# Kernel optimization log

Hardware: AMD Instinct MI355X
Metric: run time of the kernel (lower is better)

The kernel has to match this reference:

```python
import jax, jax.numpy as jnp
import numpy as np

EPS = 1e-5
NEG = -1e9

def _ln(x, g, b):
    m = x.mean(-1, keepdims=True)
    v = ((x - m) ** 2).mean(-1, keepdims=True)
    return (x - m) / jnp.sqrt(v + EPS) * g + b

def setup_inputs() -> dict:
    key = jax.random.key(0)
    ks = jax.random.split(key, 32)
    B, N, D, F, L = 2, 512, 128, 512, 3
    s = 0.05
    rn = lambda k, sh, sc=s: jax.random.normal(k, sh, jnp.float32) * sc
    inp = {
        'rel_matrix': rn(ks[0], (B, N, N, 2), 1.0),
        'pre_w': rn(ks[1], (2, D)), 'pre_b': rn(ks[2], (D,)),
        'proj_w': rn(ks[3], (2 * D, D)), 'proj_b': rn(ks[4], (D,)),
        'out_w1': rn(ks[5], (D, D)),
        'bn_g': 1.0 + rn(ks[6], (D,)), 'bn_b': rn(ks[7], (D,)),
        'bn_m': rn(ks[8], (D,)),
        'bn_v': 0.5 + jax.random.uniform(ks[9], (D,), jnp.float32),
        'out_w2': rn(ks[10], (D, D)), 'out_b2': rn(ks[11], (D,)),
        'pe': rn(ks[12], (128, D)),
        'wq': rn(ks[13], (L, D, D)), 'bq': rn(ks[14], (L, D)),
        'wk': rn(ks[15], (L, D, D)), 'bk': rn(ks[16], (L, D)),
        'wv': rn(ks[17], (L, D, D)), 'bv': rn(ks[18], (L, D)),
        'wo': rn(ks[19], (L, D, D)), 'bo': rn(ks[20], (L, D)),
        'ln1g': jnp.ones((L, D), jnp.float32), 'ln1b': jnp.zeros((L, D), jnp.float32),
        'ln2g': jnp.ones((L, D), jnp.float32), 'ln2b': jnp.zeros((L, D), jnp.float32),
        'fw1': rn(ks[21], (L, D, F)), 'fb1': rn(ks[22], (L, F)),
        'fw2': rn(ks[23], (L, F, D)), 'fb2': rn(ks[24], (L, D)),
        'mask': jax.random.randint(ks[25], (B, N), 0, 2) > 0,
        'agent_id': jax.random.randint(ks[26], (B, N), 0, 128, dtype=jnp.int32),
    }
    return inp

def reference(rel_matrix, pre_w, pre_b, proj_w, proj_b, out_w1, bn_g, bn_b, bn_m, bn_v,
              out_w2, out_b2, pe, wq, bq, wk, bk, wv, bv, wo, bo,
              ln1g, ln1b, ln2g, ln2b, fw1, fb1, fw2, fb2, mask, agent_id):
    # --- pairwise relation chain (the headroom target) ---
    # symmetric pairwise validity mask (B,N,N)
    pm = (mask[:, None, :] & mask[:, :, None]).astype(rel_matrix.dtype)
    count = jnp.maximum(pm.sum(axis=2), 1.0)  # (B,N) valid-partner counts
    x = rel_matrix @ pre_w + pre_b            # (B,N,N,D) pre_proj Linear(2->128)
    pooled = jnp.einsum('bijd,bij->bid', x, pm) / count[..., None]  # masked mean over j
    x = jnp.concatenate([x, jnp.broadcast_to(pooled[:, :, None, :], x.shape)], axis=-1)
    x = x @ proj_w + proj_b                   # Linear(256->128)
    x = jnp.einsum('bijd,bij->bid', x, pm) / count[..., None]       # masked mean over j
    # out MLP: Linear(no bias) + BatchNorm1d(eval) + ReLU + Linear
    h = x @ out_w1
    h = (h - bn_m) / jnp.sqrt(bn_v + EPS) * bn_g + bn_b
    x = jax.nn.relu(h) @ out_w2 + out_b2
    x = x + pe[agent_id]                      # agent positional embedding
    # --- 3 post-norm single-head transformer layers (eval, dropout off) ---
    kbias = jnp.where(mask, 0.0, NEG)[:, None, :]  # key padding bias (B,1,N)
    scale = 1.0 / jnp.sqrt(jnp.asarray(x.shape[-1], x.dtype))
    for l in range(3):
        q = x @ wq[l] + bq[l]
        k = x @ wk[l] + bk[l]
        v = x @ wv[l] + bv[l]
        a = jax.nn.softmax(jnp.einsum('bid,bjd->bij', q, k) * scale + kbias, axis=-1)
        att = jnp.einsum('bij,bjd->bid', a, v) @ wo[l] + bo[l]
        x = _ln(x + att, ln1g[l], ln1b[l])
        ff = jax.nn.relu(x @ fw1[l] + fb1[l]) @ fw2[l] + fb2[l]
        x = _ln(x + ff, ln2g[l], ln2b[l])
    return x
```

## Files before the change

kernel.cpp:

```cpp
#include <hip/hip_runtime.h>
#include <hip/hip_bf16.h>

typedef unsigned short u16;
typedef unsigned int u32;
typedef unsigned char u8;
typedef __attribute__((ext_vector_type(8))) short bf16x8;
typedef __attribute__((ext_vector_type(4))) float f32x4;

#define DEV __device__ __forceinline__

DEV float bf2f(u16 u) { union { u32 i; float f; } c; c.i = ((u32)u) << 16; return c.f; }
DEV u16 f2bf(float f) {
  union { float f; u32 i; } c; c.f = f;
  u32 r = c.i + 0x7FFFu + ((c.i >> 16) & 1u);
  return (u16)(r >> 16);
}
DEV u32 pk2(float lo, float hi) { return (u32)f2bf(lo) | ((u32)f2bf(hi) << 16); }
DEV float rdsrc(const void* p, int e, int isb) {
  return isb ? bf2f(((const u16*)p)[e]) : ((const float*)p)[e];
}
DEV bf16x8 as_bf(uint4 v) { union { uint4 u; bf16x8 h; } c; c.u = v; return c.h; }

static constexpr int B = 2, N = 512, D = 128, F = 512;
static constexpr int NROW = B * N;
static constexpr float EPS = 1e-5f;
static constexpr float NEG = -1e9f;
static constexpr float SCALE = 0.08838834764831845f;

#define OFF_PRE_W   0
#define OFF_PRE_B   256
#define OFF_PROJ_B  33152
#define OFF_BN_G    49664
#define OFF_BN_B    49792
#define OFF_BN_M    49920
#define OFF_BN_V    50048
#define OFF_OUT_B2  66560
#define OFF_PE      66688
#define OFF_BQ      132224
#define OFF_BK      181760
#define OFF_BV      231296
#define OFF_BO      280832
#define OFF_LN1G    281216
#define OFF_LN1B    281600
#define OFF_LN2G    281984
#define OFF_LN2B    282368
#define OFF_FB1     479360
#define OFF_FB2     677504
#define W_TOTAL     677888

static constexpr int PB_PROJ = 0;
static constexpr int PB_OW1  = 8192;
static constexpr int PB_OW2  = 16384;
static constexpr int PB_L0   = 24576;
static constexpr int PB_LSTR = 98304;
static constexpr int PB_WO   = 24576;
static constexpr int PB_FW1  = 32768;
static constexpr int PB_FW2  = 65536;
static constexpr int PTOT    = 79872;

struct NEnt { const void* s; int off, n; };
struct PEnt { const void* s1; const void* s2; int o1, o2, dst, lgn, cum; };
struct PrepArgs { NEnt nrm[19]; PEnt pk[21]; };

template<int KT>
DEV f32x4 mmaKo(const uint4* __restrict__ aPk, const uint4* __restrict__ Bp,
                int ncol, int col, int lane, int kt0) {
  f32x4 acc = {0.f, 0.f, 0.f, 0.f};
  const int sub = lane >> 4;
  #pragma unroll
  for (int kt = 0; kt < KT; ++kt) {
    const int e8 = (kt0 + kt) * 4 + sub;
    acc = __builtin_amdgcn_mfma_f32_16x16x32_bf16(
        as_bf(aPk[e8 * 16 + (lane & 15)]),
        as_bf(Bp[(size_t)e8 * ncol + col]),
        acc, 0, 0, 0);
  }
  return acc;
}

DEV void packRD(u32* aPkU, int r, int d, float v) {
  const float p = __shfl_xor(v, 1, 64);
  if (!(d & 1))
    aPkU[(((d >> 3) * 16 + r) << 2) + ((d >> 1) & 3)] = pk2(v, p);
}

DEV void packP16(u32* aPkU, int colbase, int lane, f32x4 v) {
  f32x4 p;
  #pragma unroll
  for (int g = 0; g < 4; ++g) p[g] = __shfl_xor(v[g], 1, 64);
  if (!(lane & 1)) {
    const int c = colbase + lane;
    const int e8 = c >> 3, slot = (c >> 1) & 3;
    #pragma unroll
    for (int g = 0; g < 4; ++g)
      aPkU[((e8 * 16 + g) << 2) + slot] = pk2(v[g], p[g]);
  }
}

__global__ __launch_bounds__(256) void k_prep(PrepArgs pa,
    const void* __restrict__ bnv, const void* __restrict__ maskp,
    int* __restrict__ flags, int* __restrict__ mbuf,
    float* __restrict__ W, u32* __restrict__ Wb)
{
  const int t = threadIdx.x, bid = blockIdx.x;
  __shared__ int s_nb, s_m4, s_m2;
  if (t == 0) { s_nb = 0; s_m4 = 0; s_m2 = 0; }
  __syncthreads();
  if (t < 64) {
    const u32 w = ((const u32*)bnv)[t];
    if (((w >> 8) & 0xFFu) != 0x3Fu || ((w >> 24) & 0xFFu) != 0x3Fu)
      atomicOr(&s_nb, 1);
  }
  __syncthreads();
  const int isb = s_nb ? 0 : 1;

  if (bid < 16) {
    for (int ten = 0; ten < 19; ++ten) {
      const NEnt E = pa.nrm[ten];
      for (int e = bid * 256 + t; e < E.n; e += 16 * 256)
        W[E.off + e] = rdsrc(E.s, e, isb);
    }
  } else if (bid < 511) {
    for (int g = (bid - 16) * 256 + t; g < PTOT; g += 495 * 256) {
      int ei = 0;
      #pragma unroll
      for (int k = 1; k < 21; ++k) if (g >= pa.pk[k].cum) ei = k;
      const PEnt E = pa.pk[ei];
      const int li = g - E.cum;
      const int e8 = li >> E.lgn, c = li & ((1 << E.lgn) - 1);
      float f[8];
      #pragma unroll
      for (int i = 0; i < 8; ++i) {
        const int si = ((e8 * 8 + i) << E.lgn) + c;
        f[i] = rdsrc(E.s1, E.o1 + si, isb);
        if (E.s2) f[i] += rdsrc(E.s2, E.o2 + si, isb);
      }
      uint4 w;
      w.x = pk2(f[0], f[1]); w.y = pk2(f[2], f[3]);
      w.z = pk2(f[4], f[5]); w.w = pk2(f[6], f[7]);
      ((uint4*)(Wb + E.dst))[li] = w;
    }
  } else {
    {
      const u32 w = ((const u32*)maskp)[t];
      if (!(w == 0u || w == 1u || w == 0x3F800000u)) atomicOr(&s_m4, 1);
      if (!(w == 0u || w == 1u || w == 0x10000u || w == 0x10001u ||
            w == 0x3F80u || w == 0x3F800000u || w == 0x3F803F80u)) atomicOr(&s_m2, 1);
    }
    __syncthreads();
    const int mode = (!s_m4) ? 4 : ((!s_m2) ? 2 : 1);
    if (t == 0) { flags[0] = isb; flags[1] = mode; }
    #pragma unroll
    for (int k = 0; k < 4; ++k) {
      const int e = k * 256 + t;
      int v;
      if (mode == 4)      v = (((const u32*)maskp)[e] != 0u);
      else if (mode == 2) v = (((const u16*)maskp)[e] != 0);
      else                v = (((const u8*)maskp)[e]  != 0);
      mbuf[e] = v;
    }
  }
}

__global__ __launch_bounds__(512) void k_relq(
    const void* __restrict__ relv, const float* __restrict__ W,
    const u32* __restrict__ Wb,
    const int* __restrict__ flags, const int* __restrict__ mbuf,
    const int* __restrict__ agent_id, float* __restrict__ xbuf,
    float* __restrict__ qb, u32* __restrict__ kbT, u32* __restrict__ vbT)
{
  const int t = threadIdx.x;
  const int row0 = blockIdx.x * 4;
  const int b = row0 >> 9;
  const int wid = t >> 6;
  const int lane = t & 63;

  __shared__ uint4 aPk[2][256];
  __shared__ float wred[8][9];
  __shared__ float sT0[4], sT1[4], sMt;

  u32* a0 = (u32*)&aPk[0][0];
  u32* a1 = (u32*)&aPk[1][0];

  float s0[4] = {0, 0, 0, 0}, s1[4] = {0, 0, 0, 0}, cnt;
  {
    const int j = t;
    const float m = (float)mbuf[b * N + j];
    cnt = m;
    if (flags[0]) {
      const u32* rel2 = (const u32*)relv;
      #pragma unroll
      for (int r = 0; r < 4; ++r) {
        const u32 u = rel2[(size_t)(row0 + r) * N + j];
        s0[r] += m * bf2f((u16)(u & 0xFFFFu));
        s1[r] += m * bf2f((u16)(u >> 16));
      }
    } else {
      const float2* relf = (const float2*)relv;
      #pragma unroll
      for (int r = 0; r < 4; ++r) {
        const float2 u = relf[(size_t)(row0 + r) * N + j];
        s0[r] += m * u.x; s1[r] += m * u.y;
      }
    }
  }
  if ((t & 15) >= 4) {
    const uint4 z = {0u, 0u, 0u, 0u};
    aPk[t >> 8][t & 255] = z;
  }
  #pragma unroll
  for (int o = 32; o > 0; o >>= 1) {
    #pragma unroll
    for (int r = 0; r < 4; ++r) {
      s0[r] += __shfl_xor(s0[r], o, 64);
      s1[r] += __shfl_xor(s1[r], o, 64);
    }
    cnt += __shfl_xor(cnt, o, 64);
  }
  if ((t & 63) == 0) {
    #pragma unroll
    for (int r = 0; r < 4; ++r) { wred[wid][r] = s0[r]; wred[wid][4 + r] = s1[r]; }
    wred[wid][8] = cnt;
  }
  __syncthreads();
  if (t < 4) {
    float a0v = 0, a1v = 0;
    #pragma unroll
    for (int w = 0; w < 8; ++w) { a0v += wred[w][t]; a1v += wred[w][4 + t]; }
    sT0[t] = a0v; sT1[t] = a1v;
  }
  if (t == 8) {
    float c = 0;
    #pragma unroll
    for (int w = 0; w < 8; ++w) c += wred[w][8];
    sMt = c;
  }
  __syncthreads();

  {
    const int r = t >> 7, c = t & 127;
    const int mi = mbuf[row0 + r];
    const float v = mi ? (sT0[r] * W[OFF_PRE_W + c] + sT1[r] * W[OFF_PRE_W + D + c]) / sMt
                         + W[OFF_PRE_B + c]
                       : 0.f;
    packRD(a0, r, c, v);
  }
  __syncthreads();

  {
    const int col = wid * 16 + (lane & 15);
    f32x4 acc = mmaKo<4>(&aPk[0][0], (const uint4*)(Wb + PB_PROJ), 128, col, lane, 0);
    if (lane < 16) {
      const float pb = W[OFF_PROJ_B + col];
      f32x4 v;
      #pragma unroll
      for (int g = 0; g < 4; ++g) v[g] = mbuf[row0 + g] ? acc[g] + pb : 0.f;
      packP16(a1, wid * 16, lane, v);
    }
  }
  __syncthreads();

  {
    const int col = wid * 16 + (lane & 15);
    f32x4 acc = mmaKo<4>(&aPk[1][0], (const uint4*)(Wb + PB_OW1), 128, col, lane, 0);
    if (lane < 16) {
      const float bnm = W[OFF_BN_M + col];
      const float rs  = __frsqrt_rn(W[OFF_BN_V + col] + EPS);
      const float bg  = W[OFF_BN_G + col], bb = W[OFF_BN_B + col];
      f32x4 v;
      #pragma unroll
      for (int g = 0; g < 4; ++g) v[g] = fmaxf((acc[g] - bnm) * rs * bg + bb, 0.f);
      packP16(a0, wid * 16, lane, v);
    }
  }
  __syncthreads();

  {
    const int col = wid * 16 + (lane & 15);
    f32x4 acc = mmaKo<4>(&aPk[0][0], (const uint4*)(Wb + PB_OW2), 128, col, lane, 0);
    if (lane < 16) {
      const float ob = W[OFF_OUT_B2 + col];
      f32x4 v;
      #pragma unroll
      for (int g = 0; g < 4; ++g) {
        const int aid = agent_id[row0 + g];
        v[g] = acc[g] + ob + W[OFF_PE + aid * D + col];
        xbuf[(size_t)(row0 + g) * D + col] = v[g];
      }
      packP16(a1, wid * 16, lane, v);
    }
  }
  __syncthreads();

  {
    const int col = wid * 16 + (lane & 15);
    const int i0 = row0 & 511;
    #pragma unroll
    for (int m = 0; m < 3; ++m) {
      f32x4 acc = mmaKo<4>(&aPk[1][0], (const uint4*)(Wb + PB_L0 + m * 8192), 128, col, lane, 0);
      if (lane < 16) {
        const float bb = W[(m == 0 ? OFF_BQ : m == 1 ? OFF_BK : OFF_BV) + col];
        f32x4 v;
        #pragma unroll
        for (int g = 0; g < 4; ++g) v[g] = acc[g] + bb;
        if (m == 0) {
          #pragma unroll
          for (int g = 0; g < 4; ++g) qb[(size_t)(row0 + g) * D + col] = v[g];
        } else if (m == 1) {
          f32x4 p;
          #pragma unroll
          for (int g = 0; g < 4; ++g) p[g] = __shfl_xor(v[g], 1, 64);
          if (!(lane & 1)) {
            const int e8 = col >> 3, slot = (col >> 1) & 3;
            #pragma unroll
            for (int g = 0; g < 4; ++g)
              ((u32*)kbT)[(((size_t)b * 16 + e8) * 512 + i0 + g) * 4 + slot] = pk2(v[g], p[g]);
          }
        } else {
          uint2 w;
          w.x = pk2(v[0], v[1]); w.y = pk2(v[2], v[3]);
          *(uint2*)(vbT + (((size_t)b * 64 + (i0 >> 3)) * 128 + col) * 4 + 2 * ((i0 >> 2) & 1)) = w;
        }
      }
    }
  }
}

__global__ __launch_bounds__(1024) void k_layer(
    const float* __restrict__ qin, const u32* __restrict__ kinT, const u32* __restrict__ vinT,
    const float* __restrict__ W, const u32* __restrict__ Wb, const int l, const int last,
    float* __restrict__ qout, u32* __restrict__ koutT, u32* __restrict__ voutT,
    const int* __restrict__ mbuf, float* __restrict__ xbuf, float* __restrict__ outp)
{
  const int t = threadIdx.x;
  const int row0 = blockIdx.x * 4;
  const int b = row0 >> 9;
  const int wid = t >> 6;
  const int lane = t & 63;
  const int w8 = wid & 7, half = wid >> 3;

  const uint4* WOp = (const uint4*)(Wb + PB_L0 + l * PB_LSTR + PB_WO);
  const uint4* W1p = (const uint4*)(Wb + PB_L0 + l * PB_LSTR + PB_FW1);
  const uint4* W2p = (const uint4*)(Wb + PB_L0 + l * PB_LSTR + PB_FW2);
  const float* bo  = W + OFF_BO  + l * D;
  const float* g1  = W + OFF_LN1G + l * D;
  const float* b1  = W + OFF_LN1B + l * D;
  const float* fb1 = W + OFF_FB1 + l * F;
  const float* fb2 = W + OFF_FB2 + l * D;
  const float* g2  = W + OFF_LN2G + l * D;
  const float* b2v = W + OFF_LN2B + l * D;

  __shared__ float bufA[4][512];
  __shared__ float xs[4][D];
  __shared__ float pA[4][D], pB[4][D];
  __shared__ uint4 aPk[2][1024];
  __shared__ float den[4];

  u32* a0 = (u32*)&aPk[0][0];
  u32* a1 = (u32*)&aPk[1][0];

  for (int i = t; i < 2048; i += 1024)
    if ((i & 15) >= 4) {
      const uint4 z = {0u, 0u, 0u, 0u};
      aPk[i >> 10][i & 1023] = z;
    }
  if (t < 512) {
    const int r = t >> 7, d = t & 127;
    packRD(a0, r, d, qin[(size_t)(row0 + r) * D + d] * SCALE);
  }
  __syncthreads();

  {
    const uint4* Kp = (const uint4*)kinT + (size_t)b * 16 * 512;
    #pragma unroll
    for (int ii = 0; ii < 2; ++ii) {
      const int col = (wid + 16 * ii) * 16 + (lane & 15);
      f32x4 acc = mmaKo<4>(&aPk[0][0], Kp, 512, col, lane, 0);
      if (lane < 16) {
        const float bias = mbuf[b * N + col] ? 0.f : NEG;
        #pragma unroll
        for (int g = 0; g < 4; ++g) bufA[g][col] = acc[g] + bias;
      }
    }
  }
  __syncthreads();

  if (wid < 4) {
    const int r = wid;
    float pv[8];
    float mx = -1e30f;
    #pragma unroll
    for (int k = 0; k < 8; ++k) { pv[k] = bufA[r][lane + 64 * k]; mx = fmaxf(mx, pv[k]); }
    #pragma unroll
    for (int o = 32; o > 0; o >>= 1) mx = fmaxf(mx, __shfl_xor(mx, o, 64));
    float sum = 0.f;
    #pragma unroll
    for (int k = 0; k < 8; ++k) { pv[k] = __expf(pv[k] - mx); sum += pv[k]; }
    #pragma unroll
    for (int o = 32; o > 0; o >>= 1) sum += __shfl_xor(sum, o, 64);
    #pragma unroll
    for (int k = 0; k < 8; ++k) {
      const float pp = __shfl_xor(pv[k], 1, 64);
      if (!(lane & 1)) {
        const int c = lane + 64 * k;
        a1[(((c >> 3) * 16 + r) << 2) + ((c >> 1) & 3)] = pk2(pv[k], pp);
      }
    }
    if (lane == 0) den[r] = sum;
  }
  __syncthreads();

  {
    const int col = w8 * 16 + (lane & 15);
    const uint4* Vp = (const uint4*)vinT + (size_t)b * 64 * 128;
    f32x4 acc = mmaKo<8>(&aPk[1][0], Vp, 128, col, lane, half * 8);
    if (lane < 16) {
      float* dst = half ? &pB[0][0] : &pA[0][0];
      #pragma unroll
      for (int g = 0; g < 4; ++g) dst[g * D + col] = acc[g];
    }
  }
  __syncthreads();

  if (t < 512) {
    const int r = t >> 7, d = t & 127;
    packRD(a0, r, d, (pA[r][d] + pB[r][d]) / den[r]);
  }
  __syncthreads();

  {
    const int col = w8 * 16 + (lane & 15);
    f32x4 acc = mmaKo<2>(&aPk[0][0], WOp, 128, col, lane, half * 2);
    if (lane < 16) {
      float* dst = half ? &pB[0][0] : &pA[0][0];
      #pragma unroll
      for (int g = 0; g < 4; ++g) dst[g * D + col] = acc[g];
    }
  }
  __syncthreads();

  if (wid < 4) {
    const int r = wid;
    float tv[2];
    #pragma unroll
    for (int k = 0; k < 2; ++k) {
      const int d = lane + 64 * k;
      tv[k] = pA[r][d] + pB[r][d] + bo[d] + xbuf[(size_t)(row0 + r) * D + d];
    }
    float s = tv[0] + tv[1], sq = tv[0] * tv[0] + tv[1] * tv[1];
    #pragma unroll
    for (int o = 32; o > 0; o >>= 1) { s += __shfl_xor(s, o, 64); sq += __shfl_xor(sq, o, 64); }
    const float mean = s * (1.f / 128.f);
    const float var  = sq * (1.f / 128.f) - mean * mean;
    const float rstd = __frsqrt_rn(var + EPS);
    #pragma unroll
    for (int k = 0; k < 2; ++k) {
      const int d = lane + 64 * k;
      const float xn = (tv[k] - mean) * rstd * g1[d] + b1[d];
      xs[r][d] = xn;
      const float pp = __shfl_xor(xn, 1, 64);
      if (!(lane & 1))
        a1[(((d >> 3) * 16 + r) << 2) + ((d >> 1) & 3)] = pk2(xn, pp);
    }
  }
  __syncthreads();

  {
    #pragma unroll
    for (int ii = 0; ii < 2; ++ii) {
      const int colbase = (wid + 16 * ii) * 16;
      const int col = colbase + (lane & 15);
      f32x4 acc = mmaKo<4>(&aPk[1][0], W1p, 512, col, lane, 0);
      if (lane < 16) {
        const float bb = fb1[col];
        f32x4 v;
        #pragma unroll
        for (int g = 0; g < 4; ++g) v[g] = fmaxf(acc[g] + bb, 0.f);
        packP16(a0, colbase, lane, v);
      }
    }
  }
  __syncthreads();

  {
    const int col = w8 * 16 + (lane & 15);
    f32x4 acc = mmaKo<8>(&aPk[0][0], W2p, 128, col, lane, half * 8);
    if (lane < 16) {
      float* dst = half ? &pB[0][0] : &pA[0][0];
      #pragma unroll
      for (int g = 0; g < 4; ++g) dst[g * D + col] = acc[g];
    }
  }
  __syncthreads();

  if (wid < 4) {
    const int r = wid;
    float tv[2];
    #pragma unroll
    for (int k = 0; k < 2; ++k) {
      const int d = lane + 64 * k;
      tv[k] = pA[r][d] + pB[r][d] + fb2[d] + xs[r][d];
    }
    float s = tv[0] + tv[1], sq = tv[0] * tv[0] + tv[1] * tv[1];
    #pragma unroll
    for (int o = 32; o > 0; o >>= 1) { s += __shfl_xor(s, o, 64); sq += __shfl_xor(sq, o, 64); }
    const float mean = s * (1.f / 128.f);
    const float var  = sq * (1.f / 128.f) - mean * mean;
    const float rstd = __frsqrt_rn(var + EPS);
    #pragma unroll
    for (int k = 0; k < 2; ++k) {
      const int d = lane + 64 * k;
      const float xn = (tv[k] - mean) * rstd * g2[d] + b2v[d];
      xbuf[(size_t)(row0 + r) * D + d] = xn;
      if (last) outp[(size_t)(row0 + r) * D + d] = xn;
      const float pp = __shfl_xor(xn, 1, 64);
      if (!last && !(lane & 1))
        a1[(((d >> 3) * 16 + r) << 2) + ((d >> 1) & 3)] = pk2(xn, pp);
    }
  }

  if (!last) {
    __syncthreads();
    const int i0 = row0 & 511;
    #pragma unroll
    for (int it = 0; it < 2; ++it) {
      const int task = wid + 16 * it;
      if (task < 24) {
        const int m = task >> 3, c8 = task & 7;
        const int col = c8 * 16 + (lane & 15);
        const uint4* Bp = (const uint4*)(Wb + PB_L0 + (l + 1) * PB_LSTR + m * 8192);
        f32x4 acc = mmaKo<4>(&aPk[1][0], Bp, 128, col, lane, 0);
        if (lane < 16) {
          const float bb = W[(m == 0 ? OFF_BQ : m == 1 ? OFF_BK : OFF_BV) + (l + 1) * D + col];
          f32x4 v;
          #pragma unroll
          for (int g = 0; g < 4; ++g) v[g] = acc[g] + bb;
          if (m == 0) {
            #pragma unroll
            for (int g = 0; g < 4; ++g) qout[(size_t)(row0 + g) * D + col] = v[g];
          } else if (m == 1) {
            f32x4 p;
            #pragma unroll
            for (int g = 0; g < 4; ++g) p[g] = __shfl_xor(v[g], 1, 64);
            if (!(lane & 1)) {
              const int e8 = col >> 3, slot = (col >> 1) & 3;
              #pragma unroll
              for (int g = 0; g < 4; ++g)
                ((u32*)koutT)[(((size_t)b * 16 + e8) * 512 + i0 + g) * 4 + slot] = pk2(v[g], p[g]);
            }
          } else {
            uint2 w;
            w.x = pk2(v[0], v[1]); w.y = pk2(v[2], v[3]);
            *(uint2*)(voutT + (((size_t)b * 64 + (i0 >> 3)) * 128 + col) * 4 + 2 * ((i0 >> 2) & 1)) = w;
          }
        }
      }
    }
  }
}

extern "C" void kernel_launch(void* const* d_in, const int* in_sizes, int n_in,
                              void* d_out, int out_size, void* d_ws, size_t ws_size,
                              hipStream_t stream) {
  int*   flags = (int*)d_ws;
  int*   mbuf  = flags + 16;
  float* xbuf  = (float*)d_ws + 1040;
  float* q0    = xbuf + NROW * D;
  float* q1    = q0 + NROW * D;
  u32*   kT0   = (u32*)(q1 + NROW * D);
  u32*   kT1   = kT0 + 65536;
  u32*   vT0   = kT1 + 65536;
  u32*   vT1   = vT0 + 65536;
  float* W     = (float*)(vT1 + 65536);
  u32*   Wb    = (u32*)(W + W_TOTAL);

  PrepArgs pa;
  {
    const NEnt nrm[19] = {
      {d_in[1],  OFF_PRE_W,  256}, {d_in[2],  OFF_PRE_B, 128},
      {d_in[4],  OFF_PROJ_B, 128},
      {d_in[6],  OFF_BN_G,   128}, {d_in[7],  OFF_BN_B,  128},
      {d_in[8],  OFF_BN_M,   128}, {d_in[9],  OFF_BN_V,  128},
      {d_in[11], OFF_OUT_B2, 128}, {d_in[12], OFF_PE,  16384},
      {d_in[14], OFF_BQ,     384}, {d_in[16], OFF_BK,    384},
      {d_in[18], OFF_BV,     384}, {d_in[20], OFF_BO,    384},
      {d_in[21], OFF_LN1G,   384}, {d_in[22], OFF_LN1B,  384},
      {d_in[23], OFF_LN2G,   384}, {d_in[24], OFF_LN2B,  384},
      {d_in[26], OFF_FB1,   1536}, {d_in[28], OFF_FB2,   384}};
    for (int i = 0; i < 19; ++i) pa.nrm[i] = nrm[i];

    pa.pk[0] = {d_in[3], d_in[3], 0, 16384, PB_PROJ, 7, 0};
    pa.pk[1] = {d_in[5],  nullptr, 0, 0, PB_OW1, 7, 2048};
    pa.pk[2] = {d_in[10], nullptr, 0, 0, PB_OW2, 7, 4096};
    for (int l = 0; l < 3; ++l) {
      const int lb = PB_L0 + l * PB_LSTR;
      const int cl = 6144 + l * 24576;
      pa.pk[3 + 6 * l + 0] = {d_in[13], nullptr, l * 16384, 0, lb,          7, cl};
      pa.pk[3 + 6 * l + 1] = {d_in[15], nullptr, l * 16384, 0, lb + 8192,   7, cl + 2048};
      pa.pk[3 + 6 * l + 2] = {d_in[17], nullptr, l * 16384, 0, lb + 16384,  7, cl + 4096};
      pa.pk[3 + 6 * l + 3] = {d_in[19], nullptr, l * 16384, 0, lb + PB_WO,  7, cl + 6144};
      pa.pk[3 + 6 * l + 4] = {d_in[25], nullptr, l * 65536, 0, lb + PB_FW1, 9, cl + 8192};
      pa.pk[3 + 6 * l + 5] = {d_in[27], nullptr, l * 65536, 0, lb + PB_FW2, 7, cl + 16384};
    }
  }
  const int* agent_id = (const int*)d_in[30];

  k_prep<<<512, 256, 0, stream>>>(pa, d_in[9], d_in[29], flags, mbuf, W, Wb);
  k_relq<<<NROW / 4, 512, 0, stream>>>(d_in[0], W, Wb, flags, mbuf, agent_id, xbuf,
                                       q0, kT0, vT0);

  float* qs_[2] = {q0, q1};
  u32*   ks_[2] = {kT0, kT1};
  u32*   vs_[2] = {vT0, vT1};
  for (int l = 0; l < 3; ++l) {
    const int cur = l & 1, nxt = cur ^ 1;
    const int last = (l == 2);
    k_layer<<<NROW / 4, 1024, 0, stream>>>(
        qs_[cur], ks_[cur], vs_[cur],
        W, Wb, l, last,
        qs_[nxt], ks_[nxt], vs_[nxt],
        mbuf, xbuf, last ? (float*)d_out : (float*)nullptr);
  }
}
```

Baseline: 66.63 us.

## Prefetch MFMA B operands into registers before barriers and store Q pre-packed bf16

Each matmul stage in the layer kernel now loads its weight, K and V operand fragments into registers before the preceding __syncthreads, so global-load latency overlaps the barrier and the previous stage. Q is written pre-packed in bf16 MFMA layout, so the next layer copies it straight into shared memory instead of converting and packing fp32. The softmax scale is folded into K at write time. This raises register pressure at 1024 threads per block and changes rounding order slightly, since Q and the scaled K are now rounded to bf16 separately.

```diff
diff --git a/kernel.cpp b/kernel.cpp
--- a/kernel.cpp
+++ b/kernel.cpp
@@ -78,6 +78,30 @@
   return acc;
 }
 
+template<int KT>
+DEV void loadB(const uint4* __restrict__ Bp, int ncol, int col, int lane,
+               int kt0, uint4* breg) {
+  const int sub = lane >> 4;
+  #pragma unroll
+  for (int kt = 0; kt < KT; ++kt)
+    breg[kt] = Bp[(size_t)((kt0 + kt) * 4 + sub) * ncol + col];
+}
+
+template<int KT>
+DEV f32x4 mmaR(const uint4* __restrict__ aPk, const uint4* breg, int lane, int kt0) {
+  f32x4 acc = {0.f, 0.f, 0.f, 0.f};
+  const int sub = lane >> 4;
+  #pragma unroll
+  for (int kt = 0; kt < KT; ++kt) {
+    const int e8 = (kt0 + kt) * 4 + sub;
+    acc = __builtin_amdgcn_mfma_f32_16x16x32_bf16(
+        as_bf(aPk[e8 * 16 + (lane & 15)]),
+        as_bf(breg[kt]),
+        acc, 0, 0, 0);
+  }
+  return acc;
+}
+
 DEV void packRD(u32* aPkU, int r, int d, float v) {
   const float p = __shfl_xor(v, 1, 64);
   if (!(d & 1))
@@ -167,10 +191,11 @@
     const u32* __restrict__ Wb,
     const int* __restrict__ flags, const int* __restrict__ mbuf,
     const int* __restrict__ agent_id, float* __restrict__ xbuf,
-    float* __restrict__ qb, u32* __restrict__ kbT, u32* __restrict__ vbT)
+    u32* __restrict__ qP, u32* __restrict__ kbT, u32* __restrict__ vbT)
 {
   const int t = threadIdx.x;
-  const int row0 = blockIdx.x * 4;
+  const int blk = blockIdx.x;
+  const int row0 = blk * 4;
   const int b = row0 >> 9;
   const int wid = t >> 6;
   const int lane = t & 63;
@@ -304,8 +329,15 @@
         #pragma unroll
         for (int g = 0; g < 4; ++g) v[g] = acc[g] + bb;
         if (m == 0) {
+          f32x4 p;
           #pragma unroll
-          for (int g = 0; g < 4; ++g) qb[(size_t)(row0 + g) * D + col] = v[g];
+          for (int g = 0; g < 4; ++g) p[g] = __shfl_xor(v[g], 1, 64);
+          if (!(lane & 1)) {
+            const int e8 = col >> 3, slot = (col >> 1) & 3;
+            #pragma unroll
+            for (int g = 0; g < 4; ++g)
+              qP[blk * 256 + (e8 * 4 + g) * 4 + slot] = pk2(v[g], p[g]);
+          }
         } else if (m == 1) {
           f32x4 p;
           #pragma unroll
@@ -314,7 +346,8 @@
             const int e8 = col >> 3, slot = (col >> 1) & 3;
             #pragma unroll
             for (int g = 0; g < 4; ++g)
-              ((u32*)kbT)[(((size_t)b * 16 + e8) * 512 + i0 + g) * 4 + slot] = pk2(v[g], p[g]);
+              ((u32*)kbT)[(((size_t)b * 16 + e8) * 512 + i0 + g) * 4 + slot]
+                  = pk2(v[g] * SCALE, p[g] * SCALE);
           }
         } else {
           uint2 w;
@@ -327,13 +360,14 @@
 }
 
 __global__ __launch_bounds__(1024) void k_layer(
-    const float* __restrict__ qin, const u32* __restrict__ kinT, const u32* __restrict__ vinT,
+    const u32* __restrict__ qPin, const u32* __restrict__ kinT, const u32* __restrict__ vinT,
     const float* __restrict__ W, const u32* __restrict__ Wb, const int l, const int last,
-    float* __restrict__ qout, u32* __restrict__ koutT, u32* __restrict__ voutT,
+    u32* __restrict__ qPout, u32* __restrict__ koutT, u32* __restrict__ voutT,
     const int* __restrict__ mbuf, float* __restrict__ xbuf, float* __restrict__ outp)
 {
   const int t = threadIdx.x;
-  const int row0 = blockIdx.x * 4;
+  const int blk = blockIdx.x;
+  const int row0 = blk * 4;
   const int b = row0 >> 9;
   const int wid = t >> 6;
   const int lane = t & 63;
@@ -364,18 +398,20 @@
       const uint4 z = {0u, 0u, 0u, 0u};
       aPk[i >> 10][i & 1023] = z;
     }
-  if (t < 512) {
-    const int r = t >> 7, d = t & 127;
-    packRD(a0, r, d, qin[(size_t)(row0 + r) * D + d] * SCALE);
-  }
-  __syncthreads();
-
-  {
-    const uint4* Kp = (const uint4*)kinT + (size_t)b * 16 * 512;
+  if (t < 64)
+    aPk[0][(t >> 2) * 16 + (t & 3)] = ((const uint4*)qPin)[blk * 64 + t];
+  const uint4* Kp = (const uint4*)kinT + (size_t)b * 16 * 512;
+  uint4 kB[2][4];
+  #pragma unroll
+  for (int ii = 0; ii < 2; ++ii)
+    loadB<4>(Kp, 512, (wid + 16 * ii) * 16 + (lane & 15), lane, 0, kB[ii]);
+  __syncthreads();
+
+  {
     #pragma unroll
     for (int ii = 0; ii < 2; ++ii) {
       const int col = (wid + 16 * ii) * 16 + (lane & 15);
-      f32x4 acc = mmaKo<4>(&aPk[0][0], Kp, 512, col, lane, 0);
+      f32x4 acc = mmaR<4>(&aPk[0][0], kB[ii], lane, 0);
       if (lane < 16) {
         const float bias = mbuf[b * N + col] ? 0.f : NEG;
         #pragma unroll
@@ -383,6 +419,9 @@
       }
     }
   }
+  const uint4* Vp = (const uint4*)vinT + (size_t)b * 64 * 128;
+  uint4 vB[8];
+  loadB<8>(Vp, 128, w8 * 16 + (lane & 15), lane, half * 8, vB);
   __syncthreads();
 
   if (wid < 4) {
@@ -412,14 +451,15 @@
 
   {
     const int col = w8 * 16 + (lane & 15);
-    const uint4* Vp = (const uint4*)vinT + (size_t)b * 64 * 128;
-    f32x4 acc = mmaKo<8>(&aPk[1][0], Vp, 128, col, lane, half * 8);
+    f32x4 acc = mmaR<8>(&aPk[1][0], vB, lane, half * 8);
     if (lane < 16) {
       float* dst = half ? &pB[0][0] : &pA[0][0];
       #pragma unroll
       for (int g = 0; g < 4; ++g) dst[g * D + col] = acc[g];
     }
   }
+  uint4 woB[2];
+  loadB<2>(WOp, 128, w8 * 16 + (lane & 15), lane, half * 2, woB);
   __syncthreads();
 
   if (t < 512) {
@@ -430,13 +470,17 @@
 
   {
     const int col = w8 * 16 + (lane & 15);
-    f32x4 acc = mmaKo<2>(&aPk[0][0], WOp, 128, col, lane, half * 2);
+    f32x4 acc = mmaR<2>(&aPk[0][0], woB, lane, half * 2);
     if (lane < 16) {
       float* dst = half ? &pB[0][0] : &pA[0][0];
       #pragma unroll
       for (int g = 0; g < 4; ++g) dst[g * D + col] = acc[g];
     }
   }
+  uint4 w1B[2][4];
+  #pragma unroll
+  for (int ii = 0; ii < 2; ++ii)
+    loadB<4>(W1p, 512, (wid + 16 * ii) * 16 + (lane & 15), lane, 0, w1B[ii]);
   __syncthreads();
 
   if (wid < 4) {
@@ -469,10 +513,9 @@
     #pragma unroll
     for (int ii = 0; ii < 2; ++ii) {
       const int colbase = (wid + 16 * ii) * 16;
-      const int col = colbase + (lane & 15);
-      f32x4 acc = mmaKo<4>(&aPk[1][0], W1p, 512, col, lane, 0);
+      f32x4 acc = mmaR<4>(&aPk[1][0], w1B[ii], lane, 0);
       if (lane < 16) {
-        const float bb = fb1[col];
+        const float bb = fb1[colbase + lane];
         f32x4 v;
         #pragma unroll
         for (int g = 0; g < 4; ++g) v[g] = fmaxf(acc[g] + bb, 0.f);
@@ -480,15 +523,29 @@
       }
     }
   }
+  uint4 w2B[8];
+  loadB<8>(W2p, 128, w8 * 16 + (lane & 15), lane, half * 8, w2B);
   __syncthreads();
 
   {
     const int col = w8 * 16 + (lane & 15);
-    f32x4 acc = mmaKo<8>(&aPk[0][0], W2p, 128, col, lane, half * 8);
+    f32x4 acc = mmaR<8>(&aPk[0][0], w2B, lane, half * 8);
     if (lane < 16) {
       float* dst = half ? &pB[0][0] : &pA[0][0];
       #pragma unroll
       for (int g = 0; g < 4; ++g) dst[g * D + col] = acc[g];
+    }
+  }
+  uint4 jB[2][4];
+  if (!last) {
+    #pragma unroll
+    for (int it = 0; it < 2; ++it) {
+      const int task = wid + 16 * it;
+      if (task < 24) {
+        const int m = task >> 3, c8 = task & 7;
+        const uint4* Bp = (const uint4*)(Wb + PB_L0 + (l + 1) * PB_LSTR + m * 8192);
+        loadB<4>(Bp, 128, c8 * 16 + (lane & 15), lane, 0, jB[it]);
+      }
     }
   }
   __syncthreads();
@@ -528,16 +585,22 @@
       if (task < 24) {
         const int m = task >> 3, c8 = task & 7;
         const int col = c8 * 16 + (lane & 15);
-        const uint4* Bp = (const uint4*)(Wb + PB_L0 + (l + 1) * PB_LSTR + m * 8192);
-        f32x4 acc = mmaKo<4>(&aPk[1][0], Bp, 128, col, lane, 0);
+        f32x4 acc = mmaR<4>(&aPk[1][0], jB[it], lane, 0);
         if (lane < 16) {
           const float bb = W[(m == 0 ? OFF_BQ : m == 1 ? OFF_BK : OFF_BV) + (l + 1) * D + col];
           f32x4 v;
           #pragma unroll
           for (int g = 0; g < 4; ++g) v[g] = acc[g] + bb;
           if (m == 0) {
+            f32x4 p;
             #pragma unroll
-            for (int g = 0; g < 4; ++g) qout[(size_t)(row0 + g) * D + col] = v[g];
+            for (int g = 0; g < 4; ++g) p[g] = __shfl_xor(v[g], 1, 64);
+            if (!(lane & 1)) {
+              const int e8 = col >> 3, slot = (col >> 1) & 3;
+              #pragma unroll
+              for (int g = 0; g < 4; ++g)
+                qPout[blk * 256 + (e8 * 4 + g) * 4 + slot] = pk2(v[g], p[g]);
+            }
           } else if (m == 1) {
             f32x4 p;
             #pragma unroll
@@ -546,7 +609,8 @@
               const int e8 = col >> 3, slot = (col >> 1) & 3;
               #pragma unroll
               for (int g = 0; g < 4; ++g)
-                ((u32*)koutT)[(((size_t)b * 16 + e8) * 512 + i0 + g) * 4 + slot] = pk2(v[g], p[g]);
+                ((u32*)koutT)[(((size_t)b * 16 + e8) * 512 + i0 + g) * 4 + slot]
+                    = pk2(v[g] * SCALE, p[g] * SCALE);
             }
           } else {
             uint2 w;
@@ -565,9 +629,9 @@
   int*   flags = (int*)d_ws;
   int*   mbuf  = flags + 16;
   float* xbuf  = (float*)d_ws + 1040;
-  float* q0    = xbuf + NROW * D;
-  float* q1    = q0 + NROW * D;
-  u32*   kT0   = (u32*)(q1 + NROW * D);
+  u32*   qP0   = (u32*)(xbuf + NROW * D);
+  u32*   qP1   = qP0 + 65536;
+  u32*   kT0   = qP1 + 65536;
   u32*   kT1   = kT0 + 65536;
   u32*   vT0   = kT1 + 65536;
   u32*   vT1   = vT0 + 65536;
@@ -607,11 +671,11 @@
 
   k_prep<<<512, 256, 0, stream>>>(pa, d_in[9], d_in[29], flags, mbuf, W, Wb);
   k_relq<<<NROW / 4, 512, 0, stream>>>(d_in[0], W, Wb, flags, mbuf, agent_id, xbuf,
-                                       q0, kT0, vT0);
-
-  float* qs_[2] = {q0, q1};
-  u32*   ks_[2] = {kT0, kT1};
-  u32*   vs_[2] = {vT0, vT1};
+                                       qP0, kT0, vT0);
+
+  u32* qs_[2] = {qP0, qP1};
+  u32* ks_[2] = {kT0, kT1};
+  u32* vs_[2] = {vT0, vT1};
   for (int l = 0; l < 3; ++l) {
     const int cur = l & 1, nxt = cur ^ 1;
     const int last = (l == 2);
```

Result: faster. 63.11 us (-5.3%).
